# Optimization experiments

Measured on AMD Instinct MI355X. Metric: run time of the kernel, lower is better.

Reference implementation:

```python
import jax, jax.numpy as jnp
import numpy as np

N, NODES, DIN, HID, M, OUT_FE = 8192, 20000, 768, 256, 4096, 50


def setup_inputs() -> dict:
    key = jax.random.key(0)
    ks = jax.random.split(key, 12)
    s = 0.02  # small init scale to keep tanh in its linear-ish range
    return {
        "t": jax.random.normal(ks[0], (N, DIN), jnp.float32),
        "AGE_inx": jax.random.normal(ks[1], (NODES, DIN), jnp.float32),
        "Endx": jax.random.randint(ks[2], (M,), 0, NODES, jnp.int32),
        "W_age": jax.random.normal(ks[3], (DIN, DIN), jnp.float32) * s,
        "b_age": jnp.zeros((DIN,), jnp.float32),
        "W_prjT": jax.random.normal(ks[4], (HID, DIN), jnp.float32) * s,
        "b_prjT": jnp.zeros((HID,), jnp.float32),
        "W_prjL": jax.random.normal(ks[5], (HID, DIN), jnp.float32) * s,
        "b_prjL": jnp.zeros((HID,), jnp.float32),
        "outW": jax.random.normal(ks[6], (M, HID), jnp.float32) * s,
        "outb": jax.random.normal(ks[7], (M,), jnp.float32) * s,
        "W_fc3": jax.random.normal(ks[8], (OUT_FE, HID), jnp.float32) * s,
        "b_fc3": jnp.zeros((OUT_FE,), jnp.float32),
    }


def _lintrans(x, W, b):
    # AGE LinTrans: Linear -> per-row min-max scale -> L2 normalize
    z = x @ W.T + b                                   # [NODES, 768]
    zmin = jnp.min(z, axis=1, keepdims=True)
    zmax = jnp.max(z, axis=1, keepdims=True)
    z = (z - zmin) / (zmax - zmin)
    norm = jnp.sqrt(jnp.sum(z * z, axis=1, keepdims=True))
    return z / jnp.maximum(norm, 1e-12)


def reference(t, AGE_inx, Endx, W_age, b_age, W_prjT, b_prjT,
              W_prjL, b_prjL, outW, outb, W_fc3, b_fc3):
    AGE_E = _lintrans(AGE_inx, W_age, b_age)          # [NODES, 768]
    h = jnp.tanh(t @ W_prjT.T + b_prjT)               # [N, 256]
    E = jnp.tanh(AGE_E[Endx] @ W_prjL.T + b_prjL)     # [M, 256]
    # sum_d h[n,d]*E[m,d]*outW[m,d] == h @ (E*outW).T  (avoids [N,M,256] blowup)
    o_c = h @ (E * outW).T + outb                     # [N, M]
    o_f = h @ W_fc3.T + b_fc3                         # [N, OUT_FE]
    return (o_c, o_f)
```

## Files before the change

### kernel.cpp

```cpp
#include <hip/hip_runtime.h>
#include <hip/hip_bf16.h>
#include <cstdint>
#include <cstddef>

typedef __hip_bfloat16 bf16;
typedef __attribute__((ext_vector_type(4))) float f32x4;
typedef __attribute__((ext_vector_type(8))) short s16x8;

__device__ __forceinline__ void gload_lds16(const void* g, void* l) {
    __builtin_amdgcn_global_load_lds(
        (const __attribute__((address_space(1))) unsigned int*)g,
        (__attribute__((address_space(3))) unsigned int*)l,
        16, 0, 0);
}

__global__ __launch_bounds__(256)
void cvt_f32_bf16(const float* __restrict__ src, bf16* __restrict__ dst, int n)
{
    int i = (blockIdx.x * 256 + threadIdx.x) * 4;
    if (i + 3 < n) {
        float4 v = *(const float4*)(src + i);
        dst[i + 0] = __float2bfloat16(v.x);
        dst[i + 1] = __float2bfloat16(v.y);
        dst[i + 2] = __float2bfloat16(v.z);
        dst[i + 3] = __float2bfloat16(v.w);
    }
}

__global__ __launch_bounds__(256)
void gather_cvt(const float* __restrict__ src, const int* __restrict__ idx,
                bf16* __restrict__ dst)
{
    int row = blockIdx.x;
    int r = idx[row];
    const float* s = src + (size_t)r * 768;
    bf16* d = dst + (size_t)row * 768;
    int c = threadIdx.x * 4;
    if (c < 768) {
        float4 v = *(const float4*)(s + c);
        d[c + 0] = __float2bfloat16(v.x);
        d[c + 1] = __float2bfloat16(v.y);
        d[c + 2] = __float2bfloat16(v.z);
        d[c + 3] = __float2bfloat16(v.w);
    }
}

template<int TANH, int MULW, int F32OUT, int NGUARD>
__global__ __launch_bounds__(256)
void gemm_bt(const bf16* __restrict__ A, const bf16* __restrict__ B,
             const float* __restrict__ bias, const float* __restrict__ Mul,
             void* __restrict__ Cout, int M, int N, int K, int ldc)
{
    __shared__ short sA[128 * 64];
    __shared__ short sB[128 * 64];

    const int tid  = threadIdx.x;
    const int lane = tid & 63;
    const int wave = tid >> 6;
    const int bm = blockIdx.y, bn = blockIdx.x;
    const int wr = wave >> 1, wc = wave & 1;
    const int l15 = lane & 15, quad = lane >> 4;

    f32x4 acc[4][4];
#pragma unroll
    for (int i = 0; i < 4; ++i)
#pragma unroll
        for (int j = 0; j < 4; ++j)
            acc[i][j] = (f32x4){0.f, 0.f, 0.f, 0.f};

    for (int kt = 0; kt < K; kt += 64) {
#pragma unroll
        for (int j = 0; j < 4; ++j) {
            int S   = (wave * 4 + j) * 64 + lane;
            int row = S >> 3;
            int cc  = (S & 7) ^ (row & 7);
            gload_lds16(A + (size_t)(bm * 128 + row) * K + kt + cc * 8, &sA[S * 8]);
        }
#pragma unroll
        for (int j = 0; j < 4; ++j) {
            int S   = (wave * 4 + j) * 64 + lane;
            int row = S >> 3;
            int cc  = (S & 7) ^ (row & 7);
            int ng  = bn * 128 + row;
            if (NGUARD) ng = (ng < N) ? ng : (N - 1);
            gload_lds16(B + (size_t)ng * K + kt + cc * 8, &sB[S * 8]);
        }
        asm volatile("s_waitcnt vmcnt(0)" ::: "memory");
        __syncthreads();

#pragma unroll
        for (int ks = 0; ks < 2; ++ks) {
            s16x8 afr[4], bfr[4];
#pragma unroll
            for (int i = 0; i < 4; ++i) {
                int r = wr * 64 + i * 16 + l15;
                int q = ks * 4 + quad;
                afr[i] = *(const s16x8*)&sA[(r * 8 + (q ^ (r & 7))) * 8];
            }
#pragma unroll
            for (int j = 0; j < 4; ++j) {
                int r = wc * 64 + j * 16 + l15;
                int q = ks * 4 + quad;
                bfr[j] = *(const s16x8*)&sB[(r * 8 + (q ^ (r & 7))) * 8];
            }
#pragma unroll
            for (int i = 0; i < 4; ++i)
#pragma unroll
                for (int j = 0; j < 4; ++j)
                    acc[i][j] = __builtin_amdgcn_mfma_f32_16x16x32_bf16(
                        afr[i], bfr[j], acc[i][j], 0, 0, 0);
        }
        __syncthreads();
    }

#pragma unroll
    for (int j = 0; j < 4; ++j) {
        int colg = bn * 128 + wc * 64 + j * 16 + l15;
        if (NGUARD && colg >= N) continue;
        float bv = bias[colg];
#pragma unroll
        for (int i = 0; i < 4; ++i) {
            int row0 = bm * 128 + wr * 64 + i * 16 + quad * 4;
#pragma unroll
            for (int r = 0; r < 4; ++r) {
                float v = acc[i][j][r] + bv;
                if (TANH) v = tanhf(v);
                if (MULW) v *= Mul[(size_t)(row0 + r) * N + colg];
                if (F32OUT)
                    ((float*)Cout)[(size_t)(row0 + r) * ldc + colg] = v;
                else
                    ((bf16*)Cout)[(size_t)(row0 + r) * ldc + colg] = __float2bfloat16(v);
            }
        }
    }
}

__global__ __launch_bounds__(256)
void lintrans_k(const float* __restrict__ z, bf16* __restrict__ out)
{
    __shared__ float rmin[4], rmax[4], rsum[4];
    const int row  = blockIdx.x;
    const int tid  = threadIdx.x;
    const int lane = tid & 63;
    const int wave = tid >> 6;
    const float* zr = z + (size_t)row * 768;

    float v0 = zr[tid], v1 = zr[tid + 256], v2 = zr[tid + 512];
    float mn = fminf(fminf(v0, v1), v2);
    float mx = fmaxf(fmaxf(v0, v1), v2);
#pragma unroll
    for (int o = 32; o > 0; o >>= 1) {
        mn = fminf(mn, __shfl_down(mn, o));
        mx = fmaxf(mx, __shfl_down(mx, o));
    }
    if (lane == 0) { rmin[wave] = mn; rmax[wave] = mx; }
    __syncthreads();
    float bmn = fminf(fminf(rmin[0], rmin[1]), fminf(rmin[2], rmin[3]));
    float bmx = fmaxf(fmaxf(rmax[0], rmax[1]), fmaxf(rmax[2], rmax[3]));
    float sc  = 1.f / (bmx - bmn);
    v0 = (v0 - bmn) * sc; v1 = (v1 - bmn) * sc; v2 = (v2 - bmn) * sc;
    float s = v0 * v0 + v1 * v1 + v2 * v2;
#pragma unroll
    for (int o = 32; o > 0; o >>= 1) s += __shfl_down(s, o);
    if (lane == 0) rsum[wave] = s;
    __syncthreads();
    float tot = rsum[0] + rsum[1] + rsum[2] + rsum[3];
    float inv = 1.f / fmaxf(sqrtf(tot), 1e-12f);
    out[(size_t)row * 768 + tid]       = __float2bfloat16(v0 * inv);
    out[(size_t)row * 768 + tid + 256] = __float2bfloat16(v1 * inv);
    out[(size_t)row * 768 + tid + 512] = __float2bfloat16(v2 * inv);
}

extern "C" void kernel_launch(void* const* d_in, const int* in_sizes, int n_in,
                              void* d_out, int out_size, void* d_ws, size_t ws_size,
                              hipStream_t stream)
{
    (void)in_sizes; (void)n_in; (void)out_size; (void)ws_size;

    const float* t_in   = (const float*)d_in[0];
    const float* AGEinx = (const float*)d_in[1];
    const int*   Endx   = (const int*)  d_in[2];
    const float* W_age  = (const float*)d_in[3];
    const float* b_age  = (const float*)d_in[4];
    const float* W_prjT = (const float*)d_in[5];
    const float* b_prjT = (const float*)d_in[6];
    const float* W_prjL = (const float*)d_in[7];
    const float* b_prjL = (const float*)d_in[8];
    const float* outW   = (const float*)d_in[9];
    const float* outb   = (const float*)d_in[10];
    const float* W_fc3  = (const float*)d_in[11];
    const float* b_fc3  = (const float*)d_in[12];

    char* ws = (char*)d_ws;
    size_t off = 0;
    float* z    = (float*)(ws + off);
    bf16*  h    = (bf16*)(ws + off);
    off += (size_t)4096 * 768 * 4;
    bf16* tb    = (bf16*)(ws + off); off += (size_t)8192 * 768 * 2;
    bf16* AGEg  = (bf16*)(ws + off); off += (size_t)4096 * 768 * 2;
    bf16* Wageb = (bf16*)(ws + off); off += (size_t)768 * 768 * 2;
    bf16* WpTb  = (bf16*)(ws + off); off += (size_t)256 * 768 * 2;
    bf16* WpLb  = (bf16*)(ws + off); off += (size_t)256 * 768 * 2;
    bf16* Wfc3b = (bf16*)(ws + off); off += (size_t)50 * 256 * 2 + 64;
    bf16* AGE_E = (bf16*)(ws + off); off += (size_t)4096 * 768 * 2;
    bf16* E2    = (bf16*)(ws + off); off += (size_t)4096 * 256 * 2;

    float* o_c = (float*)d_out;
    float* o_f = o_c + (size_t)8192 * 4096;

    cvt_f32_bf16<<<6144, 256, 0, stream>>>(t_in,   tb,    8192 * 768);
    cvt_f32_bf16<<<576,  256, 0, stream>>>(W_age,  Wageb, 768 * 768);
    cvt_f32_bf16<<<192,  256, 0, stream>>>(W_prjT, WpTb,  256 * 768);
    cvt_f32_bf16<<<192,  256, 0, stream>>>(W_prjL, WpLb,  256 * 768);
    cvt_f32_bf16<<<13,   256, 0, stream>>>(W_fc3,  Wfc3b, 50 * 256);
    gather_cvt  <<<4096, 256, 0, stream>>>(AGEinx, Endx,  AGEg);

    gemm_bt<0,0,1,0><<<dim3(6, 32), 256, 0, stream>>>(
        AGEg, Wageb, b_age, nullptr, z, 4096, 768, 768, 768);
    lintrans_k<<<4096, 256, 0, stream>>>(z, AGE_E);
    gemm_bt<1,1,0,0><<<dim3(2, 32), 256, 0, stream>>>(
        AGE_E, WpLb, b_prjL, outW, E2, 4096, 256, 768, 256);
    gemm_bt<1,0,0,0><<<dim3(2, 64), 256, 0, stream>>>(
        tb, WpTb, b_prjT, nullptr, h, 8192, 256, 768, 256);
    gemm_bt<0,0,1,0><<<dim3(32, 64), 256, 0, stream>>>(
        h, E2, outb, nullptr, o_c, 8192, 4096, 256, 4096);
    gemm_bt<0,0,1,1><<<dim3(1, 64), 256, 0, stream>>>(
        h, Wfc3b, b_fc3, nullptr, o_f, 8192, 50, 256, 50);
}
```

Baseline: 341.8 us.

## Merge conversion kernels and batch independent GEMMs into grouped launches

```diff
diff --git a/kernel.cpp b/kernel.cpp
--- a/kernel.cpp
+++ b/kernel.cpp
@@ -14,52 +14,20 @@
         16, 0, 0);
 }
 
-__global__ __launch_bounds__(256)
-void cvt_f32_bf16(const float* __restrict__ src, bf16* __restrict__ dst, int n)
-{
-    int i = (blockIdx.x * 256 + threadIdx.x) * 4;
-    if (i + 3 < n) {
-        float4 v = *(const float4*)(src + i);
-        dst[i + 0] = __float2bfloat16(v.x);
-        dst[i + 1] = __float2bfloat16(v.y);
-        dst[i + 2] = __float2bfloat16(v.z);
-        dst[i + 3] = __float2bfloat16(v.w);
-    }
-}
-
-__global__ __launch_bounds__(256)
-void gather_cvt(const float* __restrict__ src, const int* __restrict__ idx,
-                bf16* __restrict__ dst)
-{
-    int row = blockIdx.x;
-    int r = idx[row];
-    const float* s = src + (size_t)r * 768;
-    bf16* d = dst + (size_t)row * 768;
-    int c = threadIdx.x * 4;
-    if (c < 768) {
-        float4 v = *(const float4*)(s + c);
-        d[c + 0] = __float2bfloat16(v.x);
-        d[c + 1] = __float2bfloat16(v.y);
-        d[c + 2] = __float2bfloat16(v.z);
-        d[c + 3] = __float2bfloat16(v.w);
-    }
-}
-
-template<int TANH, int MULW, int F32OUT, int NGUARD>
-__global__ __launch_bounds__(256)
-void gemm_bt(const bf16* __restrict__ A, const bf16* __restrict__ B,
-             const float* __restrict__ bias, const float* __restrict__ Mul,
-             void* __restrict__ Cout, int M, int N, int K, int ldc)
-{
-    __shared__ short sA[128 * 64];
-    __shared__ short sB[128 * 64];
-
+struct GA {
+    const bf16* A; const bf16* B; const float* bias; const float* Mul;
+    void* C; int M, N, K, ldc, gx, cnt, flags;
+};
+
+__device__ __forceinline__ void gemm_core(short* sA, short* sB, const GA& g,
+                                          int bm, int bn)
+{
     const int tid  = threadIdx.x;
     const int lane = tid & 63;
     const int wave = tid >> 6;
-    const int bm = blockIdx.y, bn = blockIdx.x;
     const int wr = wave >> 1, wc = wave & 1;
     const int l15 = lane & 15, quad = lane >> 4;
+    const int N = g.N, K = g.K;
 
     f32x4 acc[4][4];
 #pragma unroll
@@ -74,7 +42,7 @@
             int S   = (wave * 4 + j) * 64 + lane;
             int row = S >> 3;
             int cc  = (S & 7) ^ (row & 7);
-            gload_lds16(A + (size_t)(bm * 128 + row) * K + kt + cc * 8, &sA[S * 8]);
+            gload_lds16(g.A + (size_t)(bm * 128 + row) * K + kt + cc * 8, &sA[S * 8]);
         }
 #pragma unroll
         for (int j = 0; j < 4; ++j) {
@@ -82,8 +50,8 @@
             int row = S >> 3;
             int cc  = (S & 7) ^ (row & 7);
             int ng  = bn * 128 + row;
-            if (NGUARD) ng = (ng < N) ? ng : (N - 1);
-            gload_lds16(B + (size_t)ng * K + kt + cc * 8, &sB[S * 8]);
+            ng = (ng < N) ? ng : (N - 1);
+            gload_lds16(g.B + (size_t)ng * K + kt + cc * 8, &sB[S * 8]);
         }
         asm volatile("s_waitcnt vmcnt(0)" ::: "memory");
         __syncthreads();
@@ -113,24 +81,92 @@
         __syncthreads();
     }
 
+    const bool ftanh = g.flags & 1, fmul = g.flags & 2;
+    const bool f32o  = g.flags & 4, fnt  = g.flags & 8;
 #pragma unroll
     for (int j = 0; j < 4; ++j) {
         int colg = bn * 128 + wc * 64 + j * 16 + l15;
-        if (NGUARD && colg >= N) continue;
-        float bv = bias[colg];
+        if (colg >= N) continue;
+        float bv = g.bias[colg];
 #pragma unroll
         for (int i = 0; i < 4; ++i) {
             int row0 = bm * 128 + wr * 64 + i * 16 + quad * 4;
 #pragma unroll
             for (int r = 0; r < 4; ++r) {
                 float v = acc[i][j][r] + bv;
-                if (TANH) v = tanhf(v);
-                if (MULW) v *= Mul[(size_t)(row0 + r) * N + colg];
-                if (F32OUT)
-                    ((float*)Cout)[(size_t)(row0 + r) * ldc + colg] = v;
-                else
-                    ((bf16*)Cout)[(size_t)(row0 + r) * ldc + colg] = __float2bfloat16(v);
+                if (ftanh) v = tanhf(v);
+                if (fmul)  v *= g.Mul[(size_t)(row0 + r) * N + colg];
+                size_t o = (size_t)(row0 + r) * g.ldc + colg;
+                if (f32o) {
+                    if (fnt) __builtin_nontemporal_store(v, (float*)g.C + o);
+                    else     ((float*)g.C)[o] = v;
+                } else {
+                    ((bf16*)g.C)[o] = __float2bfloat16(v);
+                }
             }
+        }
+    }
+}
+
+__global__ __launch_bounds__(256)
+void gemm_multi(GA g0, GA g1)
+{
+    __shared__ short sA[128 * 64];
+    __shared__ short sB[128 * 64];
+    int b = blockIdx.x;
+    if (b < g0.cnt) {
+        gemm_core(sA, sB, g0, b / g0.gx, b % g0.gx);
+    } else {
+        b -= g0.cnt;
+        gemm_core(sA, sB, g1, b / g1.gx, b % g1.gx);
+    }
+}
+
+__device__ __forceinline__ void cvt8(const float* s, bf16* d, int i, int n)
+{
+    if (i + 7 < n) {
+        float4 a = *(const float4*)(s + i);
+        float4 b = *(const float4*)(s + i + 4);
+        d[i + 0] = __float2bfloat16(a.x); d[i + 1] = __float2bfloat16(a.y);
+        d[i + 2] = __float2bfloat16(a.z); d[i + 3] = __float2bfloat16(a.w);
+        d[i + 4] = __float2bfloat16(b.x); d[i + 5] = __float2bfloat16(b.y);
+        d[i + 6] = __float2bfloat16(b.z); d[i + 7] = __float2bfloat16(b.w);
+    } else {
+        for (int k = i; k < n; ++k) d[k] = __float2bfloat16(s[k]);
+    }
+}
+
+__global__ __launch_bounds__(256)
+void cvt_all(const float* __restrict__ t_in,   bf16* __restrict__ tb,
+             const float* __restrict__ W_age,  bf16* __restrict__ Wageb,
+             const float* __restrict__ W_prjT, bf16* __restrict__ WpTb,
+             const float* __restrict__ W_prjL, bf16* __restrict__ WpLb,
+             const float* __restrict__ W_fc3,  bf16* __restrict__ Wfc3b,
+             const float* __restrict__ AGEinx, const int* __restrict__ Endx,
+             bf16* __restrict__ AGEg)
+{
+    int b = blockIdx.x, tid = threadIdx.x;
+    if (b < 3072)      { cvt8(t_in,   tb,    (b * 256 + tid) * 8, 8192 * 768); return; }
+    b -= 3072;
+    if (b < 288)       { cvt8(W_age,  Wageb, (b * 256 + tid) * 8, 768 * 768);  return; }
+    b -= 288;
+    if (b < 96)        { cvt8(W_prjT, WpTb,  (b * 256 + tid) * 8, 256 * 768);  return; }
+    b -= 96;
+    if (b < 96)        { cvt8(W_prjL, WpLb,  (b * 256 + tid) * 8, 256 * 768);  return; }
+    b -= 96;
+    if (b < 7)         { cvt8(W_fc3,  Wfc3b, (b * 256 + tid) * 8, 50 * 256);   return; }
+    b -= 7;
+    {
+        int r = Endx[b];
+        const float* s = AGEinx + (size_t)r * 768;
+        bf16* d = AGEg + (size_t)b * 768;
+        int c = tid * 4;
+        if (c < 768) {
+            float4 v = *(const float4*)(s + c);
+            d[c + 0] = __float2bfloat16(v.x);
+            d[c + 1] = __float2bfloat16(v.y);
+            d[c + 2] = __float2bfloat16(v.z);
+            d[c + 3] = __float2bfloat16(v.w);
         }
     }
 }
@@ -193,37 +229,35 @@
 
     char* ws = (char*)d_ws;
     size_t off = 0;
-    float* z    = (float*)(ws + off);
-    bf16*  h    = (bf16*)(ws + off);
-    off += (size_t)4096 * 768 * 4;
-    bf16* tb    = (bf16*)(ws + off); off += (size_t)8192 * 768 * 2;
-    bf16* AGEg  = (bf16*)(ws + off); off += (size_t)4096 * 768 * 2;
-    bf16* Wageb = (bf16*)(ws + off); off += (size_t)768 * 768 * 2;
-    bf16* WpTb  = (bf16*)(ws + off); off += (size_t)256 * 768 * 2;
-    bf16* WpLb  = (bf16*)(ws + off); off += (size_t)256 * 768 * 2;
-    bf16* Wfc3b = (bf16*)(ws + off); off += (size_t)50 * 256 * 2 + 64;
-    bf16* AGE_E = (bf16*)(ws + off); off += (size_t)4096 * 768 * 2;
-    bf16* E2    = (bf16*)(ws + off); off += (size_t)4096 * 256 * 2;
+    float* z    = (float*)(ws + off); off += (size_t)4096 * 768 * 4;
+    bf16*  h    = (bf16*)(ws + off);  off += (size_t)8192 * 256 * 2;
+    bf16*  tb   = (bf16*)(ws + off);  off += (size_t)8192 * 768 * 2;
+    bf16*  AGEg = (bf16*)(ws + off);  off += (size_t)4096 * 768 * 2;
+    bf16* Wageb = (bf16*)(ws + off);  off += (size_t)768 * 768 * 2;
+    bf16* WpTb  = (bf16*)(ws + off);  off += (size_t)256 * 768 * 2;
+    bf16* WpLb  = (bf16*)(ws + off);  off += (size_t)256 * 768 * 2;
+    bf16* Wfc3b = (bf16*)(ws + off);  off += (size_t)50 * 256 * 2 + 64;
+    bf16* AGE_E = (bf16*)(ws + off);  off += (size_t)4096 * 768 * 2;
+    bf16* E2    = (bf16*)(ws + off);  off += (size_t)4096 * 256 * 2;
 
     float* o_c = (float*)d_out;
     float* o_f = o_c + (size_t)8192 * 4096;
 
-    cvt_f32_bf16<<<6144, 256, 0, stream>>>(t_in,   tb,    8192 * 768);
-    cvt_f32_bf16<<<576,  256, 0, stream>>>(W_age,  Wageb, 768 * 768);
-    cvt_f32_bf16<<<192,  256, 0, stream>>>(W_prjT, WpTb,  256 * 768);
-    cvt_f32_bf16<<<192,  256, 0, stream>>>(W_prjL, WpLb,  256 * 768);
-    cvt_f32_bf16<<<13,   256, 0, stream>>>(W_fc3,  Wfc3b, 50 * 256);
-    gather_cvt  <<<4096, 256, 0, stream>>>(AGEinx, Endx,  AGEg);
-
-    gemm_bt<0,0,1,0><<<dim3(6, 32), 256, 0, stream>>>(
-        AGEg, Wageb, b_age, nullptr, z, 4096, 768, 768, 768);
+    cvt_all<<<7655, 256, 0, stream>>>(t_in, tb, W_age, Wageb, W_prjT, WpTb,
+                                      W_prjL, WpLb, W_fc3, Wfc3b,
+                                      AGEinx, Endx, AGEg);
+
+    GA g1 = { AGEg, Wageb, b_age, nullptr, z, 4096, 768, 768, 768, 6, 192, 4 };
+    GA g4 = { tb, WpTb, b_prjT, nullptr, h, 8192, 256, 768, 256, 2, 128, 1 };
+    gemm_multi<<<192 + 128, 256, 0, stream>>>(g1, g4);
+
     lintrans_k<<<4096, 256, 0, stream>>>(z, AGE_E);
-    gemm_bt<1,1,0,0><<<dim3(2, 32), 256, 0, stream>>>(
-        AGE_E, WpLb, b_prjL, outW, E2, 4096, 256, 768, 256);
-    gemm_bt<1,0,0,0><<<dim3(2, 64), 256, 0, stream>>>(
-        tb, WpTb, b_prjT, nullptr, h, 8192, 256, 768, 256);
-    gemm_bt<0,0,1,0><<<dim3(32, 64), 256, 0, stream>>>(
-        h, E2, outb, nullptr, o_c, 8192, 4096, 256, 4096);
-    gemm_bt<0,0,1,1><<<dim3(1, 64), 256, 0, stream>>>(
-        h, Wfc3b, b_fc3, nullptr, o_f, 8192, 50, 256, 50);
-}
+
+    GA g3 = { AGE_E, WpLb, b_prjL, outW, E2, 4096, 256, 768, 256, 2, 64, 3 };
+    GA g6 = { h, Wfc3b, b_fc3, nullptr, o_f, 8192, 50, 256, 50, 1, 64, 4 };
+    gemm_multi<<<64 + 64, 256, 0, stream>>>(g3, g6);
+
+    GA g5 = { h, E2, outb, nullptr, o_c, 8192, 4096, 256, 4096, 32, 2048, 4 | 8 };
+    GA gz = { nullptr, nullptr, nullptr, nullptr, nullptr, 0, 0, 0, 1, 1, 0, 0 };
+    gemm_multi<<<2048, 256, 0, stream>>>(g5, gz);
+}
```

Measured after the change: 349.8 us. 2.3% more time.
